# Kernel optimization log

Hardware: AMD Instinct MI355X
Metric: run time of the kernel (lower is better)

## Reference

```python
import jax, jax.numpy as jnp
import numpy as np

B, C, H, L = 8, 1, 512, 4096


def setup_inputs() -> dict:
    key = jax.random.key(0)
    k1, k2, k3, k4, k5 = jax.random.split(key, 5)
    u = jax.random.normal(k1, (B, H, L), dtype=jnp.float32)
    # SSM kernel k (C, H, L): stand-in for HippoSSKernel output, scaled so the
    # length-L convolution has O(1) variance.
    k = jax.random.normal(k2, (C, H, L), dtype=jnp.float32) * (1.0 / np.sqrt(L))
    D = jax.random.normal(k3, (C, H), dtype=jnp.float32)
    # output_linear: pointwise linear (C*H) -> H
    W = jax.random.normal(k4, (H, C * H), dtype=jnp.float32) * (1.0 / np.sqrt(C * H))
    b = jax.random.normal(k5, (H,), dtype=jnp.float32) * 0.01
    return {"u": u, "k": k, "D": D, "W": W, "b": b}


def reference(u, k, D, W, b):
    # u: (B, H, L), k: (C, H, L), D: (C, H), W: (H, C*H), b: (H,)
    Lq = u.shape[-1]
    n = 2 * Lq  # zero-padded FFT length for linear (non-circular) convolution
    k_f = jnp.fft.rfft(k, n=n)                       # (C, H, n//2+1) complex
    u_f = jnp.fft.rfft(u, n=n)                       # (B, H, n//2+1) complex
    y_f = jnp.einsum('bhl,chl->bchl', u_f, k_f)      # freq-domain multiply
    y = jnp.fft.irfft(y_f, n=n)[..., :Lq]            # (B, C, H, L)
    y = y + jnp.einsum('bhl,ch->bchl', u, D)         # skip term
    Bq, Cq, Hq, _ = y.shape
    y = y.reshape(Bq, Cq * Hq, Lq)                   # (B, C*H, L)
    y = jax.nn.gelu(y, approximate=False)            # torch GELU (erf)
    y = jnp.einsum('bcl,dc->bdl', y, W) + b[None, :, None]  # pointwise linear
    return y
```

## Files before the change

kernel.cpp:

```cpp
#include <hip/hip_runtime.h>
#include <hip/hip_bf16.h>
#include <math.h>

#define L_DIM 4096
#define H_DIM 512
#define B_DIM 8
#define SEG 2048

typedef __attribute__((ext_vector_type(8))) short short8;
typedef __attribute__((ext_vector_type(4))) float floatx4;

__device__ __forceinline__ unsigned f2bf(float f) {
    unsigned x = __float_as_uint(f);
    return (x + 0x7fffu + ((x >> 16) & 1u)) >> 16;
}

__global__ __launch_bounds__(256, 3) void conv_gelu_mfma(
    const float* __restrict__ u,
    const float* __restrict__ kk,
    const float* __restrict__ Dp,
    unsigned short* __restrict__ g)
{
    __shared__ __align__(16) unsigned short kA[4144];
    __shared__ __align__(16) unsigned short kB[4144];
    __shared__ __align__(16) unsigned short us[8][2104];

    const int h   = blockIdx.x;
    const int Lb  = blockIdx.y << 10;
    const int tid = threadIdx.x;
    const int lane = tid & 63;
    const int w   = tid >> 6;
    const int i   = lane & 15;
    const int q   = lane >> 4;
    const int b   = i & 7;
    const int s   = i >> 3;

    const float* kh = kk + (size_t)h * L_DIM;

    for (int p = tid; p < 4144; p += 256) {
        int t1 = L_DIM + 15 - p;
        int t2 = L_DIM + 14 - p;
        float v1 = (t1 >= 0 && t1 < L_DIM) ? kh[t1] : 0.0f;
        float v2 = (t2 >= 0 && t2 < L_DIM) ? kh[t2] : 0.0f;
        kA[p] = (unsigned short)f2bf(v1);
        kB[p] = (unsigned short)f2bf(v2);
    }

    floatx4 acc[8];
    #pragma unroll
    for (int t = 0; t < 8; t++) acc[t] = (floatx4){0.f, 0.f, 0.f, 0.f};

    const char* kbase = (const char*)((i & 1) ? kA : kB);
    const int aconst = 2 * (L_DIM + ((i & 1) ? 15 : 14) - i + 8 * q);
    const int basew = Lb + 32 * w;

    for (int seg = 0; seg < 2; seg++) {
        const int ms = seg * SEG;
        const int mstart = (seg == 0) ? -32 : SEG;
        const int segmax = ms + SEG - 32;
        if (seg == 1) {
            if (Lb + 992 < SEG) break;
            __syncthreads();
        }
        for (int e = tid * 4; e < 2096; e += 1024) {
            int m = ms - 32 + e;
            #pragma unroll
            for (int bb = 0; bb < 8; bb++) {
                float4 v = make_float4(0.f, 0.f, 0.f, 0.f);
                if (m >= 0 && m < L_DIM)
                    v = *(const float4*)(u + ((size_t)bb * H_DIM + h) * L_DIM + m);
                unsigned lo = f2bf(v.x) | (f2bf(v.y) << 16);
                unsigned hi = f2bf(v.z) | (f2bf(v.w) << 16);
                *(uint2*)&us[bb][e] = make_uint2(lo, hi);
            }
        }
        __syncthreads();

        const char* bbase = (const char*)&us[b][0] + 2 * (32 - ms + 16 * s + 8 * q);
        const char* ab = kbase + aconst;

        for (int c = 0; c < 4; c++) {
            const int c32 = 32 * c;
            const int rel = basew - c32;
            const int j_hi = (rel - mstart) >> 7;
            int j_lo = (rel - segmax + 127) >> 7;
            if (j_lo < -7) j_lo = -7;
            if (j_hi < j_lo) continue;
            const int n = j_hi - j_lo + 1;

            union AFrag { int x[4]; short8 v; };
            AFrag Wd[8];
            #pragma unroll
            for (int d = 1; d < 8; d++) {
                const int dd = c32 + (j_hi + d) * 128;
                if (dd >= 0) {
                    const int* ap = (const int*)(ab - 2 * dd);
                    Wd[d].x[0] = ap[0]; Wd[d].x[1] = ap[1];
                    Wd[d].x[2] = ap[2]; Wd[d].x[3] = ap[3];
                } else {
                    Wd[d].x[0] = 0; Wd[d].x[1] = 0; Wd[d].x[2] = 0; Wd[d].x[3] = 0;
                }
            }

            const char* aab = ab - 2 * c32 - 256 * j_hi;
            const char* bb0 = bbase + 2 * (rel - 128 * j_hi);

            for (int jb = 0; jb < n; jb += 8) {
                #pragma unroll
                for (int k = 0; k < 8; k++) {
                    const int jj = jb + k;
                    if (jj < n) {
                        const int dd0 = c32 + (j_hi - jj) * 128;
                        AFrag nf;
                        if (dd0 >= 0) {
                            const int* ap = (const int*)(aab + 256 * jj);
                            nf.x[0] = ap[0]; nf.x[1] = ap[1];
                            nf.x[2] = ap[2]; nf.x[3] = ap[3];
                        } else {
                            nf.x[0] = 0; nf.x[1] = 0; nf.x[2] = 0; nf.x[3] = 0;
                        }
                        Wd[(8 - k) & 7] = nf;
                        short8 bf = *(const short8*)(bb0 + 256 * jj);
                        #pragma unroll
                        for (int t = 0; t < 8; t++)
                            acc[t] = __builtin_amdgcn_mfma_f32_16x16x32_bf16(
                                Wd[(t - k) & 7].v, bf, acc[t], 0, 0, 0);
                    }
                }
            }
        }
    }

    const float Dh = Dp[h];
    #pragma unroll
    for (int t = 0; t < 8; t++) {
        const int l0 = Lb + 32 * w + 128 * t;
        const int lb2 = l0 + 16 * s + 4 * q;
        const size_t off = ((size_t)b * H_DIM + h) * L_DIM + lb2;
        float4 uv = *(const float4*)(u + off);
        float y0 = acc[t][0] + uv.x * Dh;
        float y1 = acc[t][1] + uv.y * Dh;
        float y2 = acc[t][2] + uv.z * Dh;
        float y3 = acc[t][3] + uv.w * Dh;
        const float c = 0.70710678118654752f;
        float g0 = 0.5f * y0 * (1.0f + erff(y0 * c));
        float g1 = 0.5f * y1 * (1.0f + erff(y1 * c));
        float g2 = 0.5f * y2 * (1.0f + erff(y2 * c));
        float g3 = 0.5f * y3 * (1.0f + erff(y3 * c));
        unsigned lo = f2bf(g0) | (f2bf(g1) << 16);
        unsigned hi = f2bf(g2) | (f2bf(g3) << 16);
        *(uint2*)(g + off) = make_uint2(lo, hi);
    }
}

__global__ __launch_bounds__(256, 2) void pointwise_mfma(
    const unsigned short* __restrict__ g,
    const float* __restrict__ W,
    const float* __restrict__ bias,
    float* __restrict__ out)
{
    __shared__ __align__(16) unsigned gs2[128 * 36];
    __shared__ __align__(16) unsigned short ws[256 * 72];

    const int tid = threadIdx.x;
    const int l0 = blockIdx.x * 128;
    const int d0 = blockIdx.y * 256;
    const int bz = blockIdx.z;
    const int w  = tid >> 6;
    const int lane = tid & 63;
    const int n  = lane & 15;
    const int q  = lane >> 4;

    const int p   = tid & 31;
    const int oct = tid >> 5;

    const int quarter = tid & 3;
    const int rb      = tid >> 2;

    floatx4 acc[8][4];
    #pragma unroll
    for (int mt = 0; mt < 8; mt++)
        #pragma unroll
        for (int nt = 0; nt < 4; nt++) acc[mt][nt] = (floatx4){0.f, 0.f, 0.f, 0.f};

    for (int c0 = 0; c0 < H_DIM; c0 += 64) {
        {
            const unsigned short* gp = g + ((size_t)bz * H_DIM + c0 + 2 * p) * L_DIM + l0 + 16 * oct;
            uint4 va0 = *(const uint4*)gp;
            uint4 va1 = *(const uint4*)(gp + 8);
            uint4 vb0 = *(const uint4*)(gp + L_DIM);
            uint4 vb1 = *(const uint4*)(gp + L_DIM + 8);
            #pragma unroll
            for (int half = 0; half < 2; half++) {
                const unsigned* ua = (const unsigned*)(half ? &va1 : &va0);
                const unsigned* ub = (const unsigned*)(half ? &vb1 : &vb0);
                #pragma unroll
                for (int e = 0; e < 4; e++) {
                    unsigned w0 = (ua[e] & 0xFFFFu) | (ub[e] << 16);
                    unsigned w1 = (ua[e] >> 16) | (ub[e] & 0xFFFF0000u);
                    const int lrow = 16 * oct + 8 * half + 2 * e;
                    gs2[lrow * 36 + p] = w0;
                    gs2[(lrow + 1) * 36 + p] = w1;
                }
            }
        }
        {
            #pragma unroll
            for (int gg = 0; gg < 4; gg++) {
                const int row = rb + 64 * gg;
                const float* wp = W + (size_t)(d0 + row) * H_DIM + c0 + 16 * quarter;
                float4 f0 = ((const float4*)wp)[0];
                float4 f1 = ((const float4*)wp)[1];
                float4 f2 = ((const float4*)wp)[2];
                float4 f3 = ((const float4*)wp)[3];
                unsigned o0 = f2bf(f0.x) | (f2bf(f0.y) << 16);
                unsigned o1 = f2bf(f0.z) | (f2bf(f0.w) << 16);
                unsigned o2 = f2bf(f1.x) | (f2bf(f1.y) << 16);
                unsigned o3 = f2bf(f1.z) | (f2bf(f1.w) << 16);
                unsigned o4 = f2bf(f2.x) | (f2bf(f2.y) << 16);
                unsigned o5 = f2bf(f2.z) | (f2bf(f2.w) << 16);
                unsigned o6 = f2bf(f3.x) | (f2bf(f3.y) << 16);
                unsigned o7 = f2bf(f3.z) | (f2bf(f3.w) << 16);
                *(uint4*)&ws[row * 72 + 16 * quarter]     = make_uint4(o0, o1, o2, o3);
                *(uint4*)&ws[row * 72 + 16 * quarter + 8] = make_uint4(o4, o5, o6, o7);
            }
        }
        __syncthreads();

        #pragma unroll
        for (int ks = 0; ks < 2; ks++) {
            short8 bfr[4];
            #pragma unroll
            for (int nt = 0; nt < 4; nt++)
                bfr[nt] = *(const short8*)&ws[(64 * w + 16 * nt + n) * 72 + 32 * ks + 8 * q];
            #pragma unroll
            for (int mt = 0; mt < 8; mt++) {
                union { uint4 u4; short8 v; } af;
                af.u4 = *(const uint4*)&gs2[(16 * mt + n) * 36 + 16 * ks + 4 * q];
                #pragma unroll
                for (int nt = 0; nt < 4; nt++)
                    acc[mt][nt] = __builtin_amdgcn_mfma_f32_16x16x32_bf16(af.v, bfr[nt], acc[mt][nt], 0, 0, 0);
            }
        }
        __syncthreads();
    }

    #pragma unroll
    for (int nt = 0; nt < 4; nt++) {
        const int d = d0 + 64 * w + 16 * nt + n;
        const float bb = bias[d];
        float* obase = out + ((size_t)bz * H_DIM + d) * L_DIM + l0 + 4 * q;
        #pragma unroll
        for (int mt = 0; mt < 8; mt++) {
            float4 r = make_float4(acc[mt][nt][0] + bb, acc[mt][nt][1] + bb,
                                   acc[mt][nt][2] + bb, acc[mt][nt][3] + bb);
            *(float4*)(obase + 16 * mt) = r;
        }
    }
}

extern "C" void kernel_launch(void* const* d_in, const int* in_sizes, int n_in,
                              void* d_out, int out_size, void* d_ws, size_t ws_size,
                              hipStream_t stream) {
    const float* u    = (const float*)d_in[0];
    const float* k    = (const float*)d_in[1];
    const float* D    = (const float*)d_in[2];
    const float* W    = (const float*)d_in[3];
    const float* bias = (const float*)d_in[4];
    float* out = (float*)d_out;
    unsigned short* g = (unsigned short*)d_ws;

    conv_gelu_mfma<<<dim3(H_DIM, L_DIM / 1024), 256, 0, stream>>>(u, k, D, g);
    pointwise_mfma<<<dim3(L_DIM / 128, H_DIM / 256, B_DIM), 256, 0, stream>>>(g, W, bias, out);
}
```

Before: 279.6 us.

## Pre-convert W to bf16 in conv kernel and specialize full MFMA chunks

The conv kernel now also converts the output-linear weight W to bf16 into workspace, one row per block. The pointwise kernel then loads bf16 W directly instead of reading fp32 and converting per tile. Separately, the inner MFMA loop is split into a main part over full groups of 8 positive-offset steps, with no per-iteration bounds or zero checks, and a guarded tail. This relies on the workspace being large enough and adds a little work to the conv kernel.

```diff
diff --git a/kernel.cpp b/kernel.cpp
--- a/kernel.cpp
+++ b/kernel.cpp
@@ -19,7 +19,9 @@
     const float* __restrict__ u,
     const float* __restrict__ kk,
     const float* __restrict__ Dp,
-    unsigned short* __restrict__ g)
+    unsigned short* __restrict__ g,
+    const float* __restrict__ W,
+    unsigned short* __restrict__ Wb)
 {
     __shared__ __align__(16) unsigned short kA[4144];
     __shared__ __align__(16) unsigned short kB[4144];
@@ -35,6 +37,13 @@
     const int b   = i & 7;
     const int s   = i >> 3;
 
+    if (Wb != nullptr && blockIdx.y == 0) {
+        const float* wsrc = W + (size_t)h * H_DIM;
+        unsigned short* wdst = Wb + (size_t)h * H_DIM;
+        wdst[tid]       = (unsigned short)f2bf(wsrc[tid]);
+        wdst[tid + 256] = (unsigned short)f2bf(wsrc[tid + 256]);
+    }
+
     const float* kh = kk + (size_t)h * L_DIM;
 
     for (int p = tid; p < 4144; p += 256) {
@@ -87,25 +96,55 @@
             if (j_lo < -7) j_lo = -7;
             if (j_hi < j_lo) continue;
             const int n = j_hi - j_lo + 1;
+            int n_pos = 0;
+            if (j_hi >= 0) n_pos = j_hi - ((j_lo > 0) ? j_lo : 0) + 1;
+            const int n_main = n_pos & ~7;
 
             union AFrag { int x[4]; short8 v; };
             AFrag Wd[8];
-            #pragma unroll
-            for (int d = 1; d < 8; d++) {
-                const int dd = c32 + (j_hi + d) * 128;
-                if (dd >= 0) {
-                    const int* ap = (const int*)(ab - 2 * dd);
+            if (j_hi >= 0) {
+                #pragma unroll
+                for (int d = 1; d < 8; d++) {
+                    const int* ap = (const int*)(ab - 2 * (c32 + (j_hi + d) * 128));
                     Wd[d].x[0] = ap[0]; Wd[d].x[1] = ap[1];
                     Wd[d].x[2] = ap[2]; Wd[d].x[3] = ap[3];
-                } else {
-                    Wd[d].x[0] = 0; Wd[d].x[1] = 0; Wd[d].x[2] = 0; Wd[d].x[3] = 0;
+                }
+            } else {
+                #pragma unroll
+                for (int d = 1; d < 8; d++) {
+                    const int dd = c32 + (j_hi + d) * 128;
+                    if (dd >= 0) {
+                        const int* ap = (const int*)(ab - 2 * dd);
+                        Wd[d].x[0] = ap[0]; Wd[d].x[1] = ap[1];
+                        Wd[d].x[2] = ap[2]; Wd[d].x[3] = ap[3];
+                    } else {
+                        Wd[d].x[0] = 0; Wd[d].x[1] = 0; Wd[d].x[2] = 0; Wd[d].x[3] = 0;
+                    }
                 }
             }
 
             const char* aab = ab - 2 * c32 - 256 * j_hi;
             const char* bb0 = bbase + 2 * (rel - 128 * j_hi);
 
-            for (int jb = 0; jb < n; jb += 8) {
+            for (int jb = 0; jb < n_main; jb += 8) {
+                const char* ap8 = aab + 256 * jb;
+                const char* bp8 = bb0 + 256 * jb;
+                #pragma unroll
+                for (int k = 0; k < 8; k++) {
+                    const int* ap = (const int*)(ap8 + 256 * k);
+                    AFrag nf;
+                    nf.x[0] = ap[0]; nf.x[1] = ap[1];
+                    nf.x[2] = ap[2]; nf.x[3] = ap[3];
+                    Wd[(8 - k) & 7] = nf;
+                    short8 bf = *(const short8*)(bp8 + 256 * k);
+                    #pragma unroll
+                    for (int t = 0; t < 8; t++)
+                        acc[t] = __builtin_amdgcn_mfma_f32_16x16x32_bf16(
+                            Wd[(t - k) & 7].v, bf, acc[t], 0, 0, 0);
+                }
+            }
+
+            for (int jb = n_main; jb < n; jb += 8) {
                 #pragma unroll
                 for (int k = 0; k < 8; k++) {
                     const int jj = jb + k;
@@ -153,8 +192,10 @@
     }
 }
 
+template <bool PREW>
 __global__ __launch_bounds__(256, 2) void pointwise_mfma(
     const unsigned short* __restrict__ g,
+    const unsigned short* __restrict__ Wb,
     const float* __restrict__ W,
     const float* __restrict__ bias,
     float* __restrict__ out)
@@ -204,7 +245,17 @@
                 }
             }
         }
-        {
+        if (PREW) {
+            #pragma unroll
+            for (int gg = 0; gg < 4; gg++) {
+                const int row = rb + 64 * gg;
+                const unsigned short* wp = Wb + (size_t)(d0 + row) * H_DIM + c0 + 16 * quarter;
+                uint4 w0 = ((const uint4*)wp)[0];
+                uint4 w1 = ((const uint4*)wp)[1];
+                *(uint4*)&ws[row * 72 + 16 * quarter]     = w0;
+                *(uint4*)&ws[row * 72 + 16 * quarter + 8] = w1;
+            }
+        } else {
             #pragma unroll
             for (int gg = 0; gg < 4; gg++) {
                 const int row = rb + 64 * gg;
@@ -270,6 +321,14 @@
     float* out = (float*)d_out;
     unsigned short* g = (unsigned short*)d_ws;
 
-    conv_gelu_mfma<<<dim3(H_DIM, L_DIM / 1024), 256, 0, stream>>>(u, k, D, g);
-    pointwise_mfma<<<dim3(L_DIM / 128, H_DIM / 256, B_DIM), 256, 0, stream>>>(g, W, bias, out);
+    const size_t g_bytes = (size_t)B_DIM * H_DIM * L_DIM * sizeof(unsigned short);
+    const size_t w_bytes = (size_t)H_DIM * H_DIM * sizeof(unsigned short);
+    const bool prew = ws_size >= g_bytes + w_bytes;
+    unsigned short* Wb = prew ? (unsigned short*)((char*)d_ws + g_bytes) : nullptr;
+
+    conv_gelu_mfma<<<dim3(H_DIM, L_DIM / 1024), 256, 0, stream>>>(u, k, D, g, W, Wb);
+    if (prew)
+        pointwise_mfma<true><<<dim3(L_DIM / 128, H_DIM / 256, B_DIM), 256, 0, stream>>>(g, Wb, W, bias, out);
+    else
+        pointwise_mfma<false><<<dim3(L_DIM / 128, H_DIM / 256, B_DIM), 256, 0, stream>>>(g, nullptr, W, bias, out);
 }
```

Result: faster. 260.4 us (-6.9%).
